# Performance work log

Hardware: AMD Instinct MI355X
Metric: run time of the kernel (lower is better)

## Reference

```python
import jax, jax.numpy as jnp
import numpy as np

IN_CAPS = 8      # I
IN_DIM = 768     # E (== D here, required by the module's reshape/matmul)
NUM_CAPS = 8     # J
DIM_CAPS = 768   # D
NUM_ROUTING = 3
EPS = 1e-8

def _pearsonr(x, y):
    # correlation along the last (capsule) dim, keepdims -> [..., 1]
    xm = x - jnp.mean(x, axis=-1, keepdims=True)
    ym = y - jnp.mean(y, axis=-1, keepdims=True)
    num = jnp.sum(xm * ym, axis=-1, keepdims=True)
    den = jnp.sqrt(jnp.sum(xm * xm, axis=-1, keepdims=True) * jnp.sum(ym * ym, axis=-1, keepdims=True))
    return num / (den + EPS)

def _squash(s):
    n2 = jnp.sum(s * s, axis=-1, keepdims=True)
    return (n2 / (1.0 + n2)) * s / jnp.sqrt(n2 + EPS)

def setup_inputs() -> dict:
    key = jax.random.key(0)
    k1, k2, k3, k4, k5 = jax.random.split(key, 5)
    m = jax.random.normal(k1, (IN_CAPS, IN_DIM), dtype=jnp.float32)
    q = jax.random.normal(k2, (400, IN_DIM), dtype=jnp.float32)
    # W built from a shared seed expanded over in_caps, as in the torch module
    W_share = 0.01 * jax.random.normal(k3, (1, NUM_CAPS, 1, DIM_CAPS, IN_DIM), dtype=jnp.float32)
    W = jnp.broadcast_to(W_share, (1, NUM_CAPS, IN_CAPS, DIM_CAPS, IN_DIM)).copy()
    b = jnp.ones((1, NUM_CAPS, IN_CAPS, DIM_CAPS), dtype=jnp.float32)
    W_n = jax.random.normal(k4, (IN_DIM, DIM_CAPS), dtype=jnp.float32)
    return {"m": m, "q": q, "W": W, "b": b, "W_n": W_n}

def reference(m, q, W, b, W_n):
    Wj = W[0]  # [J, I, D, E]
    N = q.shape[0]
    # memory projection: [I, E] @ [E, D] -> [I, D] (D == E)
    m_proj = m @ W_n
    # hat_m_ij: [1, J, I, D]
    hat_m = jnp.einsum('jide,ie->jid', Wj, m_proj)[None] + b
    # hat_q_ij: [N, J, I, D]
    hat_q = jnp.einsum('jide,ne->njid', Wj, q)
    tmp_m = jax.lax.stop_gradient(hat_m)
    tmp_q = jax.lax.stop_gradient(hat_q)
    a = jnp.zeros((N, NUM_CAPS, IN_CAPS, 1), dtype=q.dtype)
    p = jnp.tanh(_pearsonr(tmp_m, tmp_q))  # [N, J, I, 1]
    for _ in range(NUM_ROUTING - 1):
        d = jax.nn.softmax(a, axis=1)                      # over capsules J
        hat_v = jnp.sum((d + p) * tmp_m, axis=2)           # [N, J, D]
        v = _squash(hat_v)                                 # [N, J, D]
        cos = jnp.einsum('jid,njd->nji', tmp_m[0], v)[..., None]  # [N, J, I, 1]
        a = a + tmp_q * cos                                # broadcasts to [N, J, I, D]
        tmp_q = 0.5 * (tmp_q + v[:, :, None, :])
        p = jnp.tanh(_pearsonr(tmp_m, tmp_q))
    d = jax.nn.softmax(a, axis=1)
    hat_v = jnp.sum((d + p) * hat_m, axis=2)               # grads flow through hat_m here
    v_out = _squash(hat_v)                                 # [N, J, D]
    return v_out.reshape(N, -1)                            # [N, J*D]
```

## Files before the change

kernel.cpp:

```cpp
#include <hip/hip_runtime.h>
#include <math.h>

#define DD    768
#define NQ    400
#define NROWS 408
#define JD    6144
#define WSLICE 4718592
#define EPSF  1e-8f
#define K2    2304
#define K2S   1536

#define OFF_H     0
#define OFF_HM    (OFF_H + 408*6144)
#define OFF_MU    (OFF_HM + 64*768)
#define OFF_MC2   (OFF_MU + 64)
#define OFF_G     (OFF_MC2 + 64)
#define OFF_DMQ   (OFF_G + 512)
#define OFF_SQ0   (OFF_DMQ + 400*64)
#define OFF_SQ20  (OFF_SQ0 + 400*8)
#define OFF_A2    (OFF_SQ20 + 400*8)
#define OFF_B2    (OFF_A2 + 512*K2S/2)

#define FOR8(M) M(0) M(1) M(2) M(3) M(4) M(5) M(6) M(7)

typedef __attribute__((ext_vector_type(8))) short short8v;
typedef __attribute__((ext_vector_type(4))) float float4v;

__device__ inline unsigned short f2bf(float x) {
    unsigned u = __float_as_uint(x);
    u += 0x7FFF + ((u >> 16) & 1);
    return (unsigned short)(u >> 16);
}
__device__ inline float bf2f(unsigned short h) {
    return __uint_as_float(((unsigned)h) << 16);
}

__global__ __launch_bounds__(256) void k_cvt(const float* __restrict__ q,
                                             const float* __restrict__ m,
                                             const float* __restrict__ Wn,
                                             const float* __restrict__ W,
                                             unsigned short* __restrict__ A2,
                                             unsigned short* __restrict__ B2)
{
    const int bid = blockIdx.x;
    const int tid = threadIdx.x;
    if (bid < 408) {
        const int r = bid;
        unsigned short* dst = A2 + (size_t)r * K2S;
        if (r < NQ) {
            const float* src = q + (size_t)r * DD;
            #pragma unroll
            for (int u0 = 0; u0 < 3; ++u0) {
                const int u = u0 * 256 + tid;
                float x = src[u];
                unsigned short hi = f2bf(x);
                unsigned short lo = f2bf(x - bf2f(hi));
                dst[u] = hi; dst[DD + u] = lo;
            }
        } else {
            const int i = r - NQ;
            float a0 = 0.f, a1 = 0.f, a2 = 0.f;
            #pragma unroll 8
            for (int e = 0; e < DD; ++e) {
                const float mv = m[i*DD + e];
                const float* wr = Wn + (size_t)e * DD;
                a0 += mv * wr[tid];
                a1 += mv * wr[tid + 256];
                a2 += mv * wr[tid + 512];
            }
            #pragma unroll
            for (int u0 = 0; u0 < 3; ++u0) {
                const int u = u0 * 256 + tid;
                float x = (u0 == 0) ? a0 : (u0 == 1) ? a1 : a2;
                unsigned short hi = f2bf(x);
                unsigned short lo = f2bf(x - bf2f(hi));
                dst[u] = hi; dst[DD + u] = lo;
            }
        }
    } else {
        const int r0 = (bid - 408) * 4;
        #pragma unroll
        for (int rr = 0; rr < 4; ++rr) {
            const int rw = r0 + rr;
            const int jj = rw / 768;
            const int d  = rw - jj * 768;
            const float* src = W + (size_t)jj * WSLICE + (size_t)d * DD;
            unsigned short* dst = B2 + (size_t)rw * K2S;
            #pragma unroll
            for (int u0 = 0; u0 < 3; ++u0) {
                const int u = u0 * 256 + tid;
                float x = src[u];
                unsigned short hi = f2bf(x);
                unsigned short lo = f2bf(x - bf2f(hi));
                dst[u] = hi; dst[DD + u] = lo;
            }
        }
    }
}

__global__ __launch_bounds__(256) void k_gemm_mfma(const unsigned short* __restrict__ A2,
                                                   const unsigned short* __restrict__ B2,
                                                   float* __restrict__ H)
{
    __shared__ __align__(16) unsigned short lds[2][12288];
    const int tid = threadIdx.x;
    const int wv  = tid >> 6;
    const int ln  = tid & 63;
    const int c0  = blockIdx.x * 64;
    const int m0  = blockIdx.y * 128;
    const int wm  = (wv >> 1) * 64;
    const int wn  = (wv & 1) * 32;
    const unsigned short* Ap = A2 + (size_t)m0 * K2S;
    const unsigned short* Bp = B2 + (size_t)c0 * K2S;

    float4v acc[4][2];
    #pragma unroll
    for (int a = 0; a < 4; ++a)
        #pragma unroll
        for (int b = 0; b < 2; ++b)
            acc[a][b] = (float4v){0.f, 0.f, 0.f, 0.f};

#define STAGE(buf, ka, kb) {                                                      \
    _Pragma("unroll")                                                             \
    for (int qq = 0; qq < 4; ++qq) {                                              \
        const int idx = (qq << 8) + tid;                                          \
        const int row = idx >> 3;                                                 \
        const int ce  = ((idx & 7) ^ (row & 7)) << 3;                             \
        __builtin_amdgcn_global_load_lds(                                         \
            (const __attribute__((address_space(1))) void*)(Ap + (size_t)row * K2S + (ka) + ce), \
            (__attribute__((address_space(3))) void*)(&lds[buf][idx * 8]), 16, 0, 0);            \
    }                                                                             \
    _Pragma("unroll")                                                             \
    for (int qq = 0; qq < 2; ++qq) {                                              \
        const int idx = (qq << 8) + tid;                                          \
        const int row = idx >> 3;                                                 \
        const int ce  = ((idx & 7) ^ (row & 7)) << 3;                             \
        __builtin_amdgcn_global_load_lds(                                         \
            (const __attribute__((address_space(1))) void*)(Bp + (size_t)row * K2S + (kb) + ce), \
            (__attribute__((address_space(3))) void*)(&lds[buf][8192 + idx * 8]), 16, 0, 0);     \
    } }

#define COMPUTE(buf) { _Pragma("unroll")                                          \
    for (int s = 0; s < 2; ++s) {                                                 \
        short8v af[4], bf[2];                                                     \
        _Pragma("unroll")                                                         \
        for (int mi = 0; mi < 4; ++mi) {                                          \
            const int row = wm + mi * 16 + (ln & 15);                             \
            const int off = row * 64 + ((s * 32 + ((ln >> 4) * 8)) ^ ((row & 7) << 3)); \
            af[mi] = *reinterpret_cast<const short8v*>(&lds[buf][off]);           \
        }                                                                         \
        _Pragma("unroll")                                                         \
        for (int ni = 0; ni < 2; ++ni) {                                          \
            const int row = wn + ni * 16 + (ln & 15);                             \
            const int off = row * 64 + ((s * 32 + ((ln >> 4) * 8)) ^ ((row & 7) << 3)); \
            bf[ni] = *reinterpret_cast<const short8v*>(&lds[buf][8192 + off]);    \
        }                                                                         \
        _Pragma("unroll")                                                         \
        for (int mi = 0; mi < 4; ++mi)                                            \
            _Pragma("unroll")                                                     \
            for (int ni = 0; ni < 2; ++ni)                                        \
                acc[mi][ni] = __builtin_amdgcn_mfma_f32_16x16x32_bf16(af[mi], bf[ni], acc[mi][ni], 0, 0, 0); \
    } }

    STAGE(0, 0, 0);
    __syncthreads();
    int cur = 0;
    for (int k0 = 64; k0 < K2; k0 += 64) {
        const int ka = (k0 < 1536) ? k0 : k0 - 1536;
        const int kb = (k0 < 768)  ? k0 : k0 - 768;
        STAGE(cur ^ 1, ka, kb);
        COMPUTE(cur);
        __syncthreads();
        cur ^= 1;
    }
    COMPUTE(cur);
#undef STAGE
#undef COMPUTE

    #pragma unroll
    for (int mi = 0; mi < 4; ++mi) {
        #pragma unroll
        for (int r = 0; r < 4; ++r) {
            const int gr = m0 + wm + mi * 16 + (ln >> 4) * 4 + r;
            if (gr < NROWS) {
                #pragma unroll
                for (int ni = 0; ni < 2; ++ni)
                    H[(size_t)gr * JD + c0 + wn + ni * 16 + (ln & 15)] = acc[mi][ni][r];
            }
        }
    }
}

__global__ __launch_bounds__(256) void k_mid(const float* __restrict__ H,
                                             const float* __restrict__ b,
                                             float* __restrict__ hm,
                                             float* __restrict__ muM,
                                             float* __restrict__ mc2M,
                                             float* __restrict__ G,
                                             float* __restrict__ dmq,
                                             float* __restrict__ Sq0v,
                                             float* __restrict__ Sq20v)
{
    const int bid = blockIdx.x;
    const int tid = threadIdx.x;
    const int lane = tid & 63, wave = tid >> 6;
    __shared__ __align__(16) float Ms[8][768];
    __shared__ float scr[8][4];
    __shared__ float smu;

    if (bid < 64) {
        const int ji = bid;
        const int j = ji >> 3, i = ji & 7;
        float vals[3];
        float s = 0.f;
        #pragma unroll
        for (int u = 0; u < 3; ++u) {
            const int d = u * 256 + tid;
            float x = H[(size_t)(NQ + i) * JD + j * DD + d] + b[(size_t)ji * DD + d];
            hm[(size_t)ji * DD + d] = x;
            vals[u] = x;
            s += x;
        }
        #pragma unroll
        for (int off = 32; off; off >>= 1) s += __shfl_down(s, off);
        if (lane == 0) scr[0][wave] = s;
        __syncthreads();
        if (tid == 0) smu = (scr[0][0] + scr[0][1] + scr[0][2] + scr[0][3]) * (1.f / 768.f);
        __syncthreads();
        const float mu = smu;
        float s2 = 0.f;
        #pragma unroll
        for (int u = 0; u < 3; ++u) { float c = vals[u] - mu; s2 += c * c; }
        __syncthreads();
        #pragma unroll
        for (int off = 32; off; off >>= 1) s2 += __shfl_down(s2, off);
        if (lane == 0) scr[0][wave] = s2;
        __syncthreads();
        if (tid == 0) { muM[ji] = mu; mc2M[ji] = scr[0][0] + scr[0][1] + scr[0][2] + scr[0][3]; }
    } else if (bid < 128) {
        const int ji = bid - 64;
        const int j = ji >> 3, i = ji & 7;
        const float* Hj = H + j * DD;
        const float* bj = b + (size_t)(j * 8) * DD;
        const float a0 = Hj[(size_t)(NQ + i) * JD + tid]       + bj[(size_t)i * DD + tid];
        const float a1 = Hj[(size_t)(NQ + i) * JD + 256 + tid] + bj[(size_t)i * DD + 256 + tid];
        const float a2 = Hj[(size_t)(NQ + i) * JD + 512 + tid] + bj[(size_t)i * DD + 512 + tid];
#define GDOT(k) { const float* Hp = Hj + (size_t)(NQ + k) * JD + tid;            \
        const float* bp = bj + (size_t)k * DD + tid;                             \
        float acc = a0*(Hp[0]+bp[0]) + a1*(Hp[256]+bp[256]) + a2*(Hp[512]+bp[512]); \
        acc += __shfl_down(acc, 32); acc += __shfl_down(acc, 16);                \
        acc += __shfl_down(acc, 8);  acc += __shfl_down(acc, 4);                 \
        acc += __shfl_down(acc, 2);  acc += __shfl_down(acc, 1);                 \
        if (lane == 0) scr[k][wave] = acc; }
        FOR8(GDOT)
#undef GDOT
        __syncthreads();
        if (tid < 8) G[ji*8 + tid] = scr[tid][0] + scr[tid][1] + scr[tid][2] + scr[tid][3];
    } else {
        const int t = bid - 128;
        const int j = t & 7;
        const int tile = t >> 3;
        #pragma unroll
        for (int r = 0; r < 8; ++r)
            for (int c = tid; c < DD; c += 256)
                Ms[r][c] = H[(size_t)(NQ + r) * JD + j * DD + c] + b[(size_t)(j * 8 + r) * DD + c];
        __syncthreads();

        for (int nn = wave; nn < 25; nn += 4) {
            const int n = tile * 25 + nn;
            const float* qp = H + (size_t)n * JD + j * DD;
            float s = 0.f, s2 = 0.f;
#define DCL(k) float d##k = 0.f;
            FOR8(DCL)
#undef DCL
            #pragma unroll 2
            for (int c = 0; c < 12; ++c) {
                const int d = lane + 64 * c;
                const float qv = qp[d];
                s += qv; s2 += qv * qv;
#define MAC(k) d##k += qv * Ms[k][d];
                FOR8(MAC)
#undef MAC
            }
#define XR(v) { v += __shfl_xor(v, 32); v += __shfl_xor(v, 16); v += __shfl_xor(v, 8); \
                v += __shfl_xor(v, 4);  v += __shfl_xor(v, 2);  v += __shfl_xor(v, 1); }
#define XRD(k) XR(d##k)
            FOR8(XRD)
#undef XRD
            XR(s) XR(s2)
#undef XR
            if (lane == 0) {
#define ST(k) dmq[(size_t)n*64 + j*8 + k] = d##k;
                FOR8(ST)
#undef ST
                Sq0v[n*8 + j] = s;
                Sq20v[n*8 + j] = s2;
            }
        }
    }
}

__global__ __launch_bounds__(256) void k_route2(const float* __restrict__ H,
                                                const float* __restrict__ hm,
                                                const float* __restrict__ muM,
                                                const float* __restrict__ mc2M,
                                                const float* __restrict__ G,
                                                const float* __restrict__ dmq,
                                                const float* __restrict__ Sq0v,
                                                const float* __restrict__ Sq20v,
                                                float* __restrict__ out)
{
    const int n = blockIdx.x;
    const int tid = threadIdx.x;
    const int lane = tid & 63, wave = tid >> 6;
    __shared__ __align__(16) float sVv[8][768];
    __shared__ float scr[24][4];
    __shared__ float rstat[24];
    __shared__ float sDot[64];
    __shared__ float sP[64], sC1[64], sC2[64], sB1[64];

#define WRED(val, idx) { float _v = (val);                           \
    _v += __shfl_down(_v, 32); _v += __shfl_down(_v, 16);            \
    _v += __shfl_down(_v, 8);  _v += __shfl_down(_v, 4);             \
    _v += __shfl_down(_v, 2);  _v += __shfl_down(_v, 1);             \
    if (lane == 0) scr[(idx)][wave] = _v; }

#define FIN(nv) { if (tid < (nv))                                    \
    rstat[tid] = scr[tid][0] + scr[tid][1] + scr[tid][2] + scr[tid][3]; }

#define DOTLOOP() for (int t = wave; t < 64; t += 4) {               \
        const int _j = t >> 3;                                       \
        const float* Mrow = hm + (size_t)t * DD;                     \
        float acc = 0.f;                                             \
        _Pragma("unroll")                                            \
        for (int c = 0; c < 3; ++c) {                                \
            const int dd = c * 256 + lane * 4;                       \
            const float4 mv = *reinterpret_cast<const float4*>(Mrow + dd);       \
            const float4 vv = *reinterpret_cast<const float4*>(&sVv[_j][dd]);    \
            acc += mv.x*vv.x + mv.y*vv.y + mv.z*vv.z + mv.w*vv.w;    \
        }                                                            \
        acc += __shfl_down(acc, 32); acc += __shfl_down(acc, 16);    \
        acc += __shfl_down(acc, 8);  acc += __shfl_down(acc, 4);     \
        acc += __shfl_down(acc, 2);  acc += __shfl_down(acc, 1);     \
        if (lane == 0) sDot[t] = acc;                                \
    }

#define XR3(v) { v += __shfl_xor(v, 1); v += __shfl_xor(v, 2); v += __shfl_xor(v, 4); }

    float w0 = 0.f, s1 = 0.f, dotM1 = 0.f, Sq1 = 0.f, Sq21 = 0.f, mu = 0.f, mc2 = 0.f;
    if (tid < 64) {
        const int j = lane >> 3;
        mu  = muM[lane];
        mc2 = mc2M[lane];
        const float smR = 768.f * mu;
        const float dq  = dmq[(size_t)n * 64 + lane];
        const float Sq  = Sq0v[n * 8 + j];
        const float Sq2v = Sq20v[n * 8 + j];
        {
            float num  = dq - mu * Sq;
            float varq = fmaxf(Sq2v - Sq * Sq * (1.f / 768.f), 0.f);
            float den  = sqrtf(mc2 * varq) + EPSF;
            w0 = tanhf(num / den) + 0.125f;
        }
        const float* Gr = G + lane * 8;
        const int base = lane & ~7;
        float gw = 0.f;
        #pragma unroll
        for (int ii = 0; ii < 8; ++ii) gw += Gr[ii] * __shfl(w0, base + ii);
        float n2h1 = w0 * gw;  XR3(n2h1);
        float dqh1 = w0 * dq;  XR3(dqh1);
        float Sh1  = w0 * smR; XR3(Sh1);
        s1 = n2h1 / ((1.f + n2h1) * sqrtf(n2h1 + EPSF));
        float c1 = s1 * gw;
        sC1[lane] = c1;
        sB1[lane] = 0.5f * s1 * w0;
        dotM1 = 0.5f * (dq + c1);
        Sq1   = 0.5f * (Sq + s1 * Sh1);
        Sq21  = 0.25f * (Sq2v + 2.f * s1 * dqh1 + s1 * s1 * n2h1);
        float varq1 = fmaxf(Sq21 - Sq1 * Sq1 * (1.f / 768.f), 0.f);
        sP[lane] = tanhf((dotM1 - mu * Sq1) / (sqrtf(mc2 * varq1) + EPSF));
    }
    __syncthreads();

    const float* Hn = H + (size_t)n * JD + tid;
    const float* hmp = hm + tid;
    float t0[8][3], tq1[8][3], vh[8][3];
    #pragma unroll
    for (int k = 0; k < 8; ++k)
        #pragma unroll
        for (int u = 0; u < 3; ++u) {
            t0[k][u] = Hn[k * DD + u * 256];
            tq1[k][u] = 0.5f * t0[k][u];
            vh[k][u] = 0.f;
        }
    #pragma unroll 1
    for (int i = 0; i < 8; ++i) {
        float c1v[8], pv[8], b1v[8];
        #pragma unroll
        for (int k = 0; k < 8; ++k) { c1v[k] = sC1[k*8+i]; pv[k] = sP[k*8+i]; b1v[k] = sB1[k*8+i]; }
        #pragma unroll
        for (int u = 0; u < 3; ++u) {
            float x[8];
            #pragma unroll
            for (int k = 0; k < 8; ++k) x[k] = t0[k][u] * c1v[k];
            float mx = fmaxf(fmaxf(fmaxf(x[0], x[1]), fmaxf(x[2], x[3])),
                             fmaxf(fmaxf(x[4], x[5]), fmaxf(x[6], x[7])));
            float es = 0.f;
            #pragma unroll
            for (int k = 0; k < 8; ++k) { x[k] = __expf(x[k] - mx); es += x[k]; }
            float inv = 1.f / es;
            #pragma unroll
            for (int k = 0; k < 8; ++k) {
                const float mval = hmp[(size_t)(k * 8 + i) * DD + u * 256];
                vh[k][u]  += (x[k] * inv + pv[k]) * mval;
                tq1[k][u] += b1v[k] * mval;
            }
        }
    }
    #pragma unroll
    for (int k = 0; k < 8; ++k) {
        float p2 = 0.f, p1 = 0.f, p0 = 0.f;
        #pragma unroll
        for (int u = 0; u < 3; ++u) {
            sVv[k][u * 256 + tid] = vh[k][u];
            p2 += vh[k][u] * vh[k][u];
            p1 += vh[k][u];
            p0 += t0[k][u] * vh[k][u];
        }
        WRED(p2, k); WRED(p1, 8 + k); WRED(p0, 16 + k);
    }
    __syncthreads();
    DOTLOOP();
    FIN(24);
    __syncthreads();

    if (tid < 64) {
        const int j = lane >> 3;
        const float n2h2 = rstat[j];
        const float Sh2  = rstat[8 + j];
        const float dqh2 = rstat[16 + j];
        const float u = sDot[lane];
        float s2 = n2h2 / ((1.f + n2h2) * sqrtf(n2h2 + EPSF));
        float c2 = s2 * u;
        sC2[lane] = c2;
        float dotM2 = 0.5f * (dotM1 + c2);
        float w0u = w0 * u; XR3(w0u);
        float dt1h2 = 0.5f * (dqh2 + s1 * w0u);
        float Sq2_ = 0.5f * (Sq1 + s2 * Sh2);
        float Sq22 = 0.25f * Sq21 + 0.5f * s2 * dt1h2 + 0.25f * s2 * s2 * n2h2;
        float varq2 = fmaxf(Sq22 - Sq2_ * Sq2_ * (1.f / 768.f), 0.f);
        sP[lane] = tanhf((dotM2 - mu * Sq2_) / (sqrtf(mc2 * varq2) + EPSF));
    }
    __syncthreads();

    #pragma unroll
    for (int k = 0; k < 8; ++k)
        #pragma unroll
        for (int u = 0; u < 3; ++u) vh[k][u] = 0.f;
    #pragma unroll 1
    for (int i = 0; i < 8; ++i) {
        float c1v[8], c2v[8], pv[8];
        #pragma unroll
        for (int k = 0; k < 8; ++k) { c1v[k] = sC1[k*8+i]; c2v[k] = sC2[k*8+i]; pv[k] = sP[k*8+i]; }
        #pragma unroll
        for (int u = 0; u < 3; ++u) {
            float x[8];
            #pragma unroll
            for (int k = 0; k < 8; ++k) x[k] = t0[k][u] * c1v[k] + tq1[k][u] * c2v[k];
            float mx = fmaxf(fmaxf(fmaxf(x[0], x[1]), fmaxf(x[2], x[3])),
                             fmaxf(fmaxf(x[4], x[5]), fmaxf(x[6], x[7])));
            float es = 0.f;
            #pragma unroll
            for (int k = 0; k < 8; ++k) { x[k] = __expf(x[k] - mx); es += x[k]; }
            float inv = 1.f / es;
            #pragma unroll
            for (int k = 0; k < 8; ++k)
                vh[k][u] += (x[k] * inv + pv[k]) * hmp[(size_t)(k * 8 + i) * DD + u * 256];
        }
    }
    #pragma unroll
    for (int k = 0; k < 8; ++k) {
        float p2 = vh[k][0]*vh[k][0] + vh[k][1]*vh[k][1] + vh[k][2]*vh[k][2];
        WRED(p2, k);
    }
    __syncthreads();
    FIN(8);
    __syncthreads();
    float* On = out + (size_t)n * JD + tid;
    #pragma unroll
    for (int k = 0; k < 8; ++k) {
        float n2 = rstat[k];
        float sc = n2 / ((1.f + n2) * sqrtf(n2 + EPSF));
        #pragma unroll
        for (int u = 0; u < 3; ++u)
            On[k * DD + u * 256] = vh[k][u] * sc;
    }
#undef WRED
#undef FIN
#undef DOTLOOP
#undef XR3
}

extern "C" void kernel_launch(void* const* d_in, const int* in_sizes, int n_in,
                              void* d_out, int out_size, void* d_ws, size_t ws_size,
                              hipStream_t stream) {
    const float* m  = (const float*)d_in[0];
    const float* q  = (const float*)d_in[1];
    const float* W  = (const float*)d_in[2];
    const float* b  = (const float*)d_in[3];
    const float* Wn = (const float*)d_in[4];
    float* out = (float*)d_out;
    float* ws  = (float*)d_ws;

    float* H     = ws + OFF_H;
    float* hm    = ws + OFF_HM;
    float* muM   = ws + OFF_MU;
    float* mc2M  = ws + OFF_MC2;
    float* G     = ws + OFF_G;
    float* dmq   = ws + OFF_DMQ;
    float* Sq0v  = ws + OFF_SQ0;
    float* Sq20v = ws + OFF_SQ20;
    unsigned short* A2 = (unsigned short*)(ws + OFF_A2);
    unsigned short* B2 = (unsigned short*)(ws + OFF_B2);

    k_cvt<<<dim3(1944), 256, 0, stream>>>(q, m, Wn, W, A2, B2);
    k_gemm_mfma<<<dim3(96, 4), 256, 0, stream>>>(A2, B2, H);
    k_mid<<<dim3(256), 256, 0, stream>>>(H, b, hm, muM, mc2M, G, dmq, Sq0v, Sq20v);
    k_route2<<<dim3(400), 256, 0, stream>>>(H, hm, muM, mc2M, G, dmq, Sq0v, Sq20v, out);
}
```

Measured before the change: 142.6 us.

## Drop lo-part of W split-bf16, fuse q-stats into routing kernel, preload hm rows

The W operand is now converted to a single bf16 instead of a hi/lo pair, which cuts the GEMM K dimension from 2304 to 1536 and halves the B buffer. The per-query dot products and sums that k_mid used to compute into workspace are now computed inside k_route2 from the loaded H row, removing 128 k_mid blocks and their global round-trip. The DOT loop is unrolled two rows at a time and the hm values are preloaded per i iteration. The main risk is accuracy, since dropping the lo correction on W lowers the precision of every product.

Result: faster. 125.1 us, median of 2 (-12.3%).

```diff
diff --git a/kernel.cpp b/kernel.cpp
--- a/kernel.cpp
+++ b/kernel.cpp
@@ -7,18 +7,16 @@
 #define JD    6144
 #define WSLICE 4718592
 #define EPSF  1e-8f
-#define K2    2304
+#define K2E   1536
 #define K2S   1536
+#define KB2S  768
 
 #define OFF_H     0
 #define OFF_HM    (OFF_H + 408*6144)
 #define OFF_MU    (OFF_HM + 64*768)
 #define OFF_MC2   (OFF_MU + 64)
 #define OFF_G     (OFF_MC2 + 64)
-#define OFF_DMQ   (OFF_G + 512)
-#define OFF_SQ0   (OFF_DMQ + 400*64)
-#define OFF_SQ20  (OFF_SQ0 + 400*8)
-#define OFF_A2    (OFF_SQ20 + 400*8)
+#define OFF_A2    (OFF_G + 512)
 #define OFF_B2    (OFF_A2 + 512*K2S/2)
 
 #define FOR8(M) M(0) M(1) M(2) M(3) M(4) M(5) M(6) M(7)
@@ -85,14 +83,11 @@
             const int jj = rw / 768;
             const int d  = rw - jj * 768;
             const float* src = W + (size_t)jj * WSLICE + (size_t)d * DD;
-            unsigned short* dst = B2 + (size_t)rw * K2S;
+            unsigned short* dst = B2 + (size_t)rw * KB2S;
             #pragma unroll
             for (int u0 = 0; u0 < 3; ++u0) {
                 const int u = u0 * 256 + tid;
-                float x = src[u];
-                unsigned short hi = f2bf(x);
-                unsigned short lo = f2bf(x - bf2f(hi));
-                dst[u] = hi; dst[DD + u] = lo;
+                dst[u] = f2bf(src[u]);
             }
         }
     }
@@ -111,7 +106,7 @@
     const int wm  = (wv >> 1) * 64;
     const int wn  = (wv & 1) * 32;
     const unsigned short* Ap = A2 + (size_t)m0 * K2S;
-    const unsigned short* Bp = B2 + (size_t)c0 * K2S;
+    const unsigned short* Bp = B2 + (size_t)c0 * KB2S;
 
     float4v acc[4][2];
     #pragma unroll
@@ -136,7 +131,7 @@
         const int row = idx >> 3;                                                 \
         const int ce  = ((idx & 7) ^ (row & 7)) << 3;                             \
         __builtin_amdgcn_global_load_lds(                                         \
-            (const __attribute__((address_space(1))) void*)(Bp + (size_t)row * K2S + (kb) + ce), \
+            (const __attribute__((address_space(1))) void*)(Bp + (size_t)row * KB2S + (kb) + ce), \
             (__attribute__((address_space(3))) void*)(&lds[buf][8192 + idx * 8]), 16, 0, 0);     \
     } }
 
@@ -165,10 +160,9 @@
     STAGE(0, 0, 0);
     __syncthreads();
     int cur = 0;
-    for (int k0 = 64; k0 < K2; k0 += 64) {
-        const int ka = (k0 < 1536) ? k0 : k0 - 1536;
-        const int kb = (k0 < 768)  ? k0 : k0 - 768;
-        STAGE(cur ^ 1, ka, kb);
+    for (int k0 = 64; k0 < K2E; k0 += 64) {
+        const int kb = (k0 < 768) ? k0 : k0 - 768;
+        STAGE(cur ^ 1, k0, kb);
         COMPUTE(cur);
         __syncthreads();
         cur ^= 1;
@@ -196,15 +190,11 @@
                                              float* __restrict__ hm,
                                              float* __restrict__ muM,
                                              float* __restrict__ mc2M,
-                                             float* __restrict__ G,
-                                             float* __restrict__ dmq,
-                                             float* __restrict__ Sq0v,
-                                             float* __restrict__ Sq20v)
+                                             float* __restrict__ G)
 {
     const int bid = blockIdx.x;
     const int tid = threadIdx.x;
     const int lane = tid & 63, wave = tid >> 6;
-    __shared__ __align__(16) float Ms[8][768];
     __shared__ float scr[8][4];
     __shared__ float smu;
 
@@ -237,7 +227,7 @@
         if (lane == 0) scr[0][wave] = s2;
         __syncthreads();
         if (tid == 0) { muM[ji] = mu; mc2M[ji] = scr[0][0] + scr[0][1] + scr[0][2] + scr[0][3]; }
-    } else if (bid < 128) {
+    } else {
         const int ji = bid - 64;
         const int j = ji >> 3, i = ji & 7;
         const float* Hj = H + j * DD;
@@ -256,47 +246,6 @@
 #undef GDOT
         __syncthreads();
         if (tid < 8) G[ji*8 + tid] = scr[tid][0] + scr[tid][1] + scr[tid][2] + scr[tid][3];
-    } else {
-        const int t = bid - 128;
-        const int j = t & 7;
-        const int tile = t >> 3;
-        #pragma unroll
-        for (int r = 0; r < 8; ++r)
-            for (int c = tid; c < DD; c += 256)
-                Ms[r][c] = H[(size_t)(NQ + r) * JD + j * DD + c] + b[(size_t)(j * 8 + r) * DD + c];
-        __syncthreads();
-
-        for (int nn = wave; nn < 25; nn += 4) {
-            const int n = tile * 25 + nn;
-            const float* qp = H + (size_t)n * JD + j * DD;
-            float s = 0.f, s2 = 0.f;
-#define DCL(k) float d##k = 0.f;
-            FOR8(DCL)
-#undef DCL
-            #pragma unroll 2
-            for (int c = 0; c < 12; ++c) {
-                const int d = lane + 64 * c;
-                const float qv = qp[d];
-                s += qv; s2 += qv * qv;
-#define MAC(k) d##k += qv * Ms[k][d];
-                FOR8(MAC)
-#undef MAC
-            }
-#define XR(v) { v += __shfl_xor(v, 32); v += __shfl_xor(v, 16); v += __shfl_xor(v, 8); \
-                v += __shfl_xor(v, 4);  v += __shfl_xor(v, 2);  v += __shfl_xor(v, 1); }
-#define XRD(k) XR(d##k)
-            FOR8(XRD)
-#undef XRD
-            XR(s) XR(s2)
-#undef XR
-            if (lane == 0) {
-#define ST(k) dmq[(size_t)n*64 + j*8 + k] = d##k;
-                FOR8(ST)
-#undef ST
-                Sq0v[n*8 + j] = s;
-                Sq20v[n*8 + j] = s2;
-            }
-        }
     }
 }
 
@@ -305,9 +254,6 @@
                                                 const float* __restrict__ muM,
                                                 const float* __restrict__ mc2M,
                                                 const float* __restrict__ G,
-                                                const float* __restrict__ dmq,
-                                                const float* __restrict__ Sq0v,
-                                                const float* __restrict__ Sq20v,
                                                 float* __restrict__ out)
 {
     const int n = blockIdx.x;
@@ -328,24 +274,57 @@
 #define FIN(nv) { if (tid < (nv))                                    \
     rstat[tid] = scr[tid][0] + scr[tid][1] + scr[tid][2] + scr[tid][3]; }
 
-#define DOTLOOP() for (int t = wave; t < 64; t += 4) {               \
-        const int _j = t >> 3;                                       \
-        const float* Mrow = hm + (size_t)t * DD;                     \
-        float acc = 0.f;                                             \
-        _Pragma("unroll")                                            \
-        for (int c = 0; c < 3; ++c) {                                \
-            const int dd = c * 256 + lane * 4;                       \
-            const float4 mv = *reinterpret_cast<const float4*>(Mrow + dd);       \
-            const float4 vv = *reinterpret_cast<const float4*>(&sVv[_j][dd]);    \
-            acc += mv.x*vv.x + mv.y*vv.y + mv.z*vv.z + mv.w*vv.w;    \
-        }                                                            \
-        acc += __shfl_down(acc, 32); acc += __shfl_down(acc, 16);    \
-        acc += __shfl_down(acc, 8);  acc += __shfl_down(acc, 4);     \
-        acc += __shfl_down(acc, 2);  acc += __shfl_down(acc, 1);     \
-        if (lane == 0) sDot[t] = acc;                                \
+#define DOT2() _Pragma("unroll 1")                                    \
+    for (int tt = 0; tt < 8; ++tt) {                                  \
+        const int ta = wave + tt * 8;                                 \
+        const int tb = ta + 4;                                        \
+        const int ja = ta >> 3, jb = tb >> 3;                         \
+        const float* Ma = hm + (size_t)ta * DD;                       \
+        const float* Mb = hm + (size_t)tb * DD;                       \
+        float4 va[3], vb[3], sa[3], sb[3];                            \
+        _Pragma("unroll")                                             \
+        for (int c = 0; c < 3; ++c) {                                 \
+            const int dd = c * 256 + lane * 4;                        \
+            va[c] = *reinterpret_cast<const float4*>(Ma + dd);        \
+            vb[c] = *reinterpret_cast<const float4*>(Mb + dd);        \
+            sa[c] = *reinterpret_cast<const float4*>(&sVv[ja][dd]);   \
+            sb[c] = *reinterpret_cast<const float4*>(&sVv[jb][dd]);   \
+        }                                                             \
+        float acca = 0.f, accb = 0.f;                                 \
+        _Pragma("unroll")                                             \
+        for (int c = 0; c < 3; ++c) {                                 \
+            acca += va[c].x*sa[c].x + va[c].y*sa[c].y + va[c].z*sa[c].z + va[c].w*sa[c].w; \
+            accb += vb[c].x*sb[c].x + vb[c].y*sb[c].y + vb[c].z*sb[c].z + vb[c].w*sb[c].w; \
+        }                                                             \
+        acca += __shfl_down(acca, 32); acca += __shfl_down(acca, 16); \
+        acca += __shfl_down(acca, 8);  acca += __shfl_down(acca, 4);  \
+        acca += __shfl_down(acca, 2);  acca += __shfl_down(acca, 1);  \
+        accb += __shfl_down(accb, 32); accb += __shfl_down(accb, 16); \
+        accb += __shfl_down(accb, 8);  accb += __shfl_down(accb, 4);  \
+        accb += __shfl_down(accb, 2);  accb += __shfl_down(accb, 1);  \
+        if (lane == 0) { sDot[ta] = acca; sDot[tb] = accb; }          \
     }
 
 #define XR3(v) { v += __shfl_xor(v, 1); v += __shfl_xor(v, 2); v += __shfl_xor(v, 4); }
+
+    const float* Hn = H + (size_t)n * JD + tid;
+    const float* hmp = hm + tid;
+    float t0[8][3], tq1[8][3], vh[8][3];
+    #pragma unroll
+    for (int k = 0; k < 8; ++k) {
+        float s = 0.f, s2 = 0.f;
+        #pragma unroll
+        for (int u = 0; u < 3; ++u) {
+            t0[k][u] = Hn[k * DD + u * 256];
+            sVv[k][u * 256 + tid] = t0[k][u];
+            s += t0[k][u]; s2 += t0[k][u] * t0[k][u];
+        }
+        WRED(s, k); WRED(s2, 8 + k);
+    }
+    __syncthreads();
+    DOT2();
+    FIN(16);
+    __syncthreads();
 
     float w0 = 0.f, s1 = 0.f, dotM1 = 0.f, Sq1 = 0.f, Sq21 = 0.f, mu = 0.f, mc2 = 0.f;
     if (tid < 64) {
@@ -353,9 +332,9 @@
         mu  = muM[lane];
         mc2 = mc2M[lane];
         const float smR = 768.f * mu;
-        const float dq  = dmq[(size_t)n * 64 + lane];
-        const float Sq  = Sq0v[n * 8 + j];
-        const float Sq2v = Sq20v[n * 8 + j];
+        const float dq  = sDot[lane];
+        const float Sq  = rstat[j];
+        const float Sq2v = rstat[8 + j];
         {
             float num  = dq - mu * Sq;
             float varq = fmaxf(Sq2v - Sq * Sq * (1.f / 768.f), 0.f);
@@ -382,19 +361,22 @@
     }
     __syncthreads();
 
-    const float* Hn = H + (size_t)n * JD + tid;
-    const float* hmp = hm + tid;
-    float t0[8][3], tq1[8][3], vh[8][3];
     #pragma unroll
     for (int k = 0; k < 8; ++k)
         #pragma unroll
         for (int u = 0; u < 3; ++u) {
-            t0[k][u] = Hn[k * DD + u * 256];
             tq1[k][u] = 0.5f * t0[k][u];
             vh[k][u] = 0.f;
         }
     #pragma unroll 1
     for (int i = 0; i < 8; ++i) {
+        const float* hb = hmp + (size_t)i * DD;
+        float mv[8][3];
+        #pragma unroll
+        for (int k = 0; k < 8; ++k)
+            #pragma unroll
+            for (int u = 0; u < 3; ++u)
+                mv[k][u] = hb[(size_t)(k * 8) * DD + u * 256];
         float c1v[8], pv[8], b1v[8];
         #pragma unroll
         for (int k = 0; k < 8; ++k) { c1v[k] = sC1[k*8+i]; pv[k] = sP[k*8+i]; b1v[k] = sB1[k*8+i]; }
@@ -411,12 +393,12 @@
             float inv = 1.f / es;
             #pragma unroll
             for (int k = 0; k < 8; ++k) {
-                const float mval = hmp[(size_t)(k * 8 + i) * DD + u * 256];
-                vh[k][u]  += (x[k] * inv + pv[k]) * mval;
-                tq1[k][u] += b1v[k] * mval;
+                vh[k][u]  += (x[k] * inv + pv[k]) * mv[k][u];
+                tq1[k][u] += b1v[k] * mv[k][u];
             }
         }
     }
+    __syncthreads();
     #pragma unroll
     for (int k = 0; k < 8; ++k) {
         float p2 = 0.f, p1 = 0.f, p0 = 0.f;
@@ -430,7 +412,8 @@
         WRED(p2, k); WRED(p1, 8 + k); WRED(p0, 16 + k);
     }
     __syncthreads();
-    DOTLOOP();
+
+    DOT2();
     FIN(24);
     __syncthreads();
 
@@ -459,6 +442,13 @@
         for (int u = 0; u < 3; ++u) vh[k][u] = 0.f;
     #pragma unroll 1
     for (int i = 0; i < 8; ++i) {
+        const float* hb = hmp + (size_t)i * DD;
+        float mv[8][3];
+        #pragma unroll
+        for (int k = 0; k < 8; ++k)
+            #pragma unroll
+            for (int u = 0; u < 3; ++u)
+                mv[k][u] = hb[(size_t)(k * 8) * DD + u * 256];
         float c1v[8], c2v[8], pv[8];
         #pragma unroll
         for (int k = 0; k < 8; ++k) { c1v[k] = sC1[k*8+i]; c2v[k] = sC2[k*8+i]; pv[k] = sP[k*8+i]; }
@@ -475,7 +465,7 @@
             float inv = 1.f / es;
             #pragma unroll
             for (int k = 0; k < 8; ++k)
-                vh[k][u] += (x[k] * inv + pv[k]) * hmp[(size_t)(k * 8 + i) * DD + u * 256];
+                vh[k][u] += (x[k] * inv + pv[k]) * mv[k][u];
         }
     }
     #pragma unroll
@@ -497,7 +487,7 @@
     }
 #undef WRED
 #undef FIN
-#undef DOTLOOP
+#undef DOT2
 #undef XR3
 }
 
@@ -517,14 +507,11 @@
     float* muM   = ws + OFF_MU;
     float* mc2M  = ws + OFF_MC2;
     float* G     = ws + OFF_G;
-    float* dmq   = ws + OFF_DMQ;
-    float* Sq0v  = ws + OFF_SQ0;
-    float* Sq20v = ws + OFF_SQ20;
     unsigned short* A2 = (unsigned short*)(ws + OFF_A2);
     unsigned short* B2 = (unsigned short*)(ws + OFF_B2);
 
     k_cvt<<<dim3(1944), 256, 0, stream>>>(q, m, Wn, W, A2, B2);
     k_gemm_mfma<<<dim3(96, 4), 256, 0, stream>>>(A2, B2, H);
-    k_mid<<<dim3(256), 256, 0, stream>>>(H, b, hm, muM, mc2M, G, dmq, Sq0v, Sq20v);
-    k_route2<<<dim3(400), 256, 0, stream>>>(H, hm, muM, mc2M, G, dmq, Sq0v, Sq20v, out);
-}
+    k_mid<<<dim3(128), 256, 0, stream>>>(H, b, hm, muM, mc2M, G);
+    k_route2<<<dim3(400), 256, 0, stream>>>(H, hm, muM, mc2M, G, out);
+}
```
